# Kernel tuning notes

Hardware: AMD Instinct MI355X
Metric: run time of the kernel (lower is better)

## Reference

```python
import jax, jax.numpy as jnp
import numpy as np

D_MODEL = 1024
NUM_HEADS = 16
HEAD_DIM = D_MODEL // NUM_HEADS
SCALE = 1.0 / np.sqrt(HEAD_DIM).astype(np.float32)


def setup_inputs() -> dict:
    key = jax.random.key(0)
    k1, k2, k3, k4 = jax.random.split(key, 4)
    B, L = 1, 4096
    s = 0.02
    x = jax.random.normal(k1, (B, L, D_MODEL), dtype=jnp.float32)
    W_qkv = jax.random.normal(k2, (D_MODEL, 3 * D_MODEL), dtype=jnp.float32) * s
    W_o = jax.random.normal(k3, (D_MODEL, D_MODEL), dtype=jnp.float32) * s
    b_o = jax.random.normal(k4, (D_MODEL,), dtype=jnp.float32) * s
    return {"x": x, "W_qkv": W_qkv, "W_o": W_o, "b_o": b_o}


def reference(x, W_qkv, W_o, b_o):
    B, L, D = x.shape
    H, Hd = NUM_HEADS, HEAD_DIM
    qkv = x @ W_qkv                          # [B, L, 3D]
    qkv = qkv.reshape(B, L, 3, H, Hd)
    q = jnp.transpose(qkv[:, :, 0], (0, 2, 1, 3))  # [B, H, L, Hd]
    k = jnp.transpose(qkv[:, :, 1], (0, 2, 1, 3))
    v = jnp.transpose(qkv[:, :, 2], (0, 2, 1, 3))
    scores = jnp.einsum("bhqd,bhkd->bhqk", q, k) * SCALE  # [B, H, L, L]
    attn = jax.nn.softmax(scores, axis=-1)
    out = jnp.einsum("bhqk,bhkd->bhqd", attn, v)          # [B, H, L, Hd]
    out = jnp.transpose(out, (0, 2, 1, 3)).reshape(B, L, D)
    return out @ W_o + b_o
```

## Files before the change

### kernel.cpp

```cpp
#include <hip/hip_runtime.h>
#include <stdint.h>


#define L_SEQ 4096
#define DM 1024
#define NHEAD 16
#define HDIM 64
#define ATT_SCALE 0.125f
#define LOG2E 1.4426950408889634f
#define CSC (ATT_SCALE * LOG2E)

typedef __attribute__((ext_vector_type(8))) __bf16 bf16x8;
typedef __attribute__((ext_vector_type(4))) __bf16 bf16x4;
typedef __attribute__((ext_vector_type(4))) float f32x4;
typedef __attribute__((ext_vector_type(8))) float f32x8;
typedef __attribute__((ext_vector_type(4))) short short4v;
typedef __attribute__((ext_vector_type(8))) short short8v;

#define GLL16(g, l) __builtin_amdgcn_global_load_lds( \
    (__attribute__((address_space(1))) void*)(g),     \
    (__attribute__((address_space(3))) void*)(l), 16, 0, 0)

#define MFMA32(a, b, c) __builtin_amdgcn_mfma_f32_16x16x32_bf16((a), (b), (c), 0, 0, 0)

__device__ __forceinline__ short f2bf(float f) {
  uint32_t u = __builtin_bit_cast(uint32_t, f);
  u += 0x7fffu + ((u >> 16) & 1u);
  return (short)(u >> 16);
}

__global__ __launch_bounds__(256)
void prep_kernel(const float* __restrict__ x, short* __restrict__ xb,
                 const float* __restrict__ Wq, short* __restrict__ wqt,
                 const float* __restrict__ Wo, short* __restrict__ wot) {
  __shared__ __align__(16) short tbuf[64 * 66];
  const int tid = threadIdx.x;
  const int blk = blockIdx.x;
  if (blk < 4096) {
    int i = blk * 256 + tid;
    float4 v = ((const float4*)x)[i];
    short4 o;
    o.x = f2bf(v.x); o.y = f2bf(v.y); o.z = f2bf(v.z); o.w = f2bf(v.w);
    ((short4*)xb)[i] = o;
    return;
  }
  const float* W; short* Wt; int N, nb, kb;
  const int K = 1024;
  if (blk < 4096 + 768) {
    int b = blk - 4096;
    W = Wq; Wt = wqt; N = 3072; nb = (b % 48) * 64; kb = (b / 48) * 64;
  } else {
    int b = blk - (4096 + 768);
    W = Wo; Wt = wot; N = 1024; nb = (b % 16) * 64; kb = (b / 16) * 64;
  }
#pragma unroll
  for (int i = 0; i < 16; i++) {
    int idx = tid + i * 256;
    int r = idx >> 6, c = idx & 63;
    tbuf[r * 66 + c] = f2bf(W[(size_t)(kb + r) * N + nb + c]);
  }
  __syncthreads();
#pragma unroll
  for (int i = 0; i < 16; i++) {
    int idx = tid + i * 256;
    int r = idx >> 6, c = idx & 63;
    Wt[(size_t)(nb + r) * K + kb + c] = tbuf[c * 66 + r];
  }
}

__global__ __launch_bounds__(256, 2)
void gemm_qkv(const short* __restrict__ A, const short* __restrict__ Bt,
              short* __restrict__ qkv, short* __restrict__ vtout, int K) {
  __shared__ __align__(16) short As[4096];
  __shared__ __align__(16) short Bs[4096];
  const int tid = threadIdx.x;
  const int lane = tid & 63;
  const int wave = tid >> 6;
  const int quad = lane >> 4;
  const int cl = lane & 15;
  const int m0 = blockIdx.x * 128;
  const int n0 = blockIdx.y * 128;
  const int wm = (wave >> 1) * 64;
  const int wn = (wave & 1) * 64;

  f32x4 acc[4][4] = {};

  for (int kb = 0; kb < K; kb += 32) {
    __syncthreads();
#pragma unroll
    for (int i = 0; i < 2; i++) {
      int ci = i * 256 + tid;
      int row = ci & 127, c = ci >> 7;
      GLL16(A + (size_t)(m0 + row) * K + kb + c * 8, As + ci * 8);
      GLL16(Bt + (size_t)(n0 + row) * K + kb + c * 8, Bs + ci * 8);
    }
    __syncthreads();
    bf16x8 af[4], bfr[4];
#pragma unroll
    for (int t = 0; t < 4; t++) {
      af[t]  = *(const bf16x8*)(As + (quad * 128 + wm + t * 16 + cl) * 8);
      bfr[t] = *(const bf16x8*)(Bs + (quad * 128 + wn + t * 16 + cl) * 8);
    }
#pragma unroll
    for (int mt = 0; mt < 4; mt++)
#pragma unroll
      for (int nt = 0; nt < 4; nt++)
        acc[mt][nt] = MFMA32(af[mt], bfr[nt], acc[mt][nt]);
  }

#pragma unroll
  for (int mt = 0; mt < 4; mt++)
#pragma unroll
    for (int nt = 0; nt < 4; nt++) {
      int col = n0 + wn + nt * 16 + cl;
      int which = col >> 10, hd = col & 63;
      int hidx = (col >> 6) & 15;
      int row0 = m0 + wm + mt * 16 + quad * 4;
      if (which == 2) {
        short4v pk;
#pragma unroll
        for (int r = 0; r < 4; r++) pk[r] = f2bf(acc[mt][nt][r]);
        *(short4v*)(vtout + ((size_t)hidx * HDIM + hd) * L_SEQ + row0) = pk;
      } else {
        float sc = (which == 0) ? CSC : 1.0f;
        size_t base = (((size_t)which * NHEAD + hidx) * L_SEQ) * HDIM + hd;
#pragma unroll
        for (int r = 0; r < 4; r++)
          qkv[base + (size_t)(row0 + r) * HDIM] = f2bf(acc[mt][nt][r] * sc);
      }
    }
}

__global__ __launch_bounds__(256, 2)
void gemm_out(const short* __restrict__ A, const short* __restrict__ Bt,
              float* __restrict__ C, const float* __restrict__ bias, int K) {
  __shared__ __align__(16) short As[4096];
  __shared__ __align__(16) short Bs[2048];
  const int tid = threadIdx.x;
  const int lane = tid & 63;
  const int wave = tid >> 6;
  const int quad = lane >> 4;
  const int cl = lane & 15;
  const int m0 = blockIdx.x * 128;
  const int n0 = blockIdx.y * 64;
  const int wm = (wave >> 1) * 64;
  const int wn = (wave & 1) * 32;
  const int N = 1024;

  f32x4 acc[4][2] = {};

  for (int kb = 0; kb < K; kb += 32) {
    __syncthreads();
#pragma unroll
    for (int i = 0; i < 2; i++) {
      int ci = i * 256 + tid;
      GLL16(A + (size_t)(m0 + (ci & 127)) * K + kb + (ci >> 7) * 8, As + ci * 8);
    }
    GLL16(Bt + (size_t)(n0 + (tid & 63)) * K + kb + (tid >> 6) * 8, Bs + tid * 8);
    __syncthreads();
    bf16x8 af[4], bfr[2];
#pragma unroll
    for (int t = 0; t < 4; t++)
      af[t] = *(const bf16x8*)(As + (quad * 128 + wm + t * 16 + cl) * 8);
#pragma unroll
    for (int t = 0; t < 2; t++)
      bfr[t] = *(const bf16x8*)(Bs + (quad * 64 + wn + t * 16 + cl) * 8);
#pragma unroll
    for (int mt = 0; mt < 4; mt++)
#pragma unroll
      for (int nt = 0; nt < 2; nt++)
        acc[mt][nt] = MFMA32(af[mt], bfr[nt], acc[mt][nt]);
  }

#pragma unroll
  for (int mt = 0; mt < 4; mt++)
#pragma unroll
    for (int nt = 0; nt < 2; nt++) {
      int col = n0 + wn + nt * 16 + cl;
      float b = bias[col];
#pragma unroll
      for (int r = 0; r < 4; r++) {
        int row = m0 + wm + mt * 16 + quad * 4 + r;
        C[(size_t)row * N + col] = acc[mt][nt][r] + b;
      }
    }
}

#define KVB 128
__global__ __launch_bounds__(512, 4)
void attn_kernel(const short* __restrict__ qkv, const short* __restrict__ vt,
                 short* __restrict__ aout) {
  __shared__ __align__(16) short Ks[2][KVB * HDIM];
  __shared__ __align__(16) short Vs[2][HDIM * KVB];
  __shared__ float lbuf[512];
  const int tid = threadIdx.x, lane = tid & 63, wave = tid >> 6;
  const int quad = lane >> 4, cl = lane & 15;
  const int kg = wave & 1;
  const int qg = wave >> 1;
  const int bid = blockIdx.x;
  const int h  = ((bid & 7) << 1) | ((bid >> 3) & 1);
  const int qb = bid >> 4;
  const short* Qg = qkv + (size_t)h * L_SEQ * HDIM;
  const short* Kg = qkv + ((size_t)NHEAD + h) * L_SEQ * HDIM;
  const short* Vg = vt + (size_t)h * HDIM * L_SEQ;
  const int keyoff = ((cl >> 2) << 3) | (cl & 3);

  bf16x8 qf[2][2];
#pragma unroll
  for (int qs = 0; qs < 2; qs++) {
    int qrow = qb * 128 + qg * 32 + qs * 16 + cl;
    qf[qs][0] = *(const bf16x8*)(Qg + (size_t)qrow * HDIM + quad * 8);
    qf[qs][1] = *(const bf16x8*)(Qg + (size_t)qrow * HDIM + 32 + quad * 8);
  }
  const short8v ov = {0x3F80, 0x3F80, 0x3F80, 0x3F80, 0x3F80, 0x3F80, 0x3F80, 0x3F80};
  const bf16x8 ones = __builtin_bit_cast(bf16x8, ov);
  f32x4 o_l[2] = {};
  f32x4 o_acc[4][2] = {};

  int koff[2][2][2];
  int voff[2][4];
#pragma unroll
  for (int kslab = 0; kslab < 2; kslab++) {
#pragma unroll
    for (int b = 0; b < 2; b++) {
      int krow = kg * 64 + kslab * 32 + keyoff + b * 4;
      int sw = (krow & 3) | (((krow >> 3) & 1) << 2);
#pragma unroll
      for (int ks = 0; ks < 2; ks++)
        koff[kslab][b][ks] = (krow * 8 + ((ks * 4 + quad) ^ sw)) * 8;
    }
#pragma unroll
    for (int G = 0; G < 4; G++) {
      int vrow = G * 16 + cl;
      int sw = (vrow & 3) | (((vrow >> 3) & 1) << 2);
      voff[kslab][G] = (vrow * 16 + ((kg * 8 + kslab * 4 + quad) ^ sw)) * 8;
    }
  }

  const short* kp[2]; const short* vp[2]; int ldsoK[2], ldsoV[2];
#pragma unroll
  for (int i = 0; i < 2; i++) {
    int ciK = i * 512 + tid;
    int rowK = ciK >> 3;
    int swK = (rowK & 3) | (((rowK >> 3) & 1) << 2);
    int cK = (ciK & 7) ^ swK;
    kp[i] = Kg + (size_t)rowK * HDIM + cK * 8;
    ldsoK[i] = ciK * 8;
    int ciV = i * 512 + tid;
    int rowV = ciV >> 4;
    int swV = (rowV & 3) | (((rowV >> 3) & 1) << 2);
    int cV = (ciV & 15) ^ swV;
    vp[i] = Vg + (size_t)rowV * L_SEQ + cV * 8;
    ldsoV[i] = ciV * 8;
  }
#define STAGE(t, buf)                                        \
  {                                                          \
    _Pragma("unroll")                                        \
    for (int i = 0; i < 2; i++) {                            \
      GLL16(kp[i] + (t) * KVB * HDIM, &Ks[buf][ldsoK[i]]);   \
      GLL16(vp[i] + (t) * KVB, &Vs[buf][ldsoV[i]]);          \
    }                                                        \
  }

  STAGE(0, 0);
#pragma unroll 2
  for (int t = 0; t < L_SEQ / KVB; t++) {
    const int cur = t & 1;
    __syncthreads();
    if (t + 1 < L_SEQ / KVB) STAGE(t + 1, cur ^ 1);
    const short* Kb = Ks[cur];
    const short* Vb = Vs[cur];

#pragma unroll
    for (int kslab = 0; kslab < 2; kslab++) {
      f32x4 s[2][2] = {};
      __builtin_amdgcn_s_setprio(1);
#pragma unroll
      for (int b = 0; b < 2; b++)
#pragma unroll
        for (int ks = 0; ks < 2; ks++) {
          bf16x8 kf = *(const bf16x8*)(Kb + koff[kslab][b][ks]);
#pragma unroll
          for (int qs = 0; qs < 2; qs++)
            s[qs][b] = MFMA32(kf, qf[qs][ks], s[qs][b]);
        }
      __builtin_amdgcn_s_setprio(0);

      bf16x8 vfr[4];
#pragma unroll
      for (int G = 0; G < 4; G++)
        vfr[G] = *(const bf16x8*)(Vb + voff[kslab][G]);

      bf16x8 pb0;
      {
        f32x8 pv8;
#pragma unroll
        for (int b = 0; b < 2; b++)
#pragma unroll
          for (int r = 0; r < 4; r++)
            pv8[b * 4 + r] = __builtin_amdgcn_exp2f(s[0][b][r]);
        pb0 = __builtin_convertvector(pv8, bf16x8);
      }

      __builtin_amdgcn_s_setprio(1);
      o_l[0] = MFMA32(ones, pb0, o_l[0]);
#pragma unroll
      for (int G = 0; G < 4; G++)
        o_acc[G][0] = MFMA32(vfr[G], pb0, o_acc[G][0]);
      __builtin_amdgcn_s_setprio(0);

      bf16x8 pb1;
      {
        f32x8 pv8;
#pragma unroll
        for (int b = 0; b < 2; b++)
#pragma unroll
          for (int r = 0; r < 4; r++)
            pv8[b * 4 + r] = __builtin_amdgcn_exp2f(s[1][b][r]);
        pb1 = __builtin_convertvector(pv8, bf16x8);
      }

      __builtin_amdgcn_s_setprio(1);
      o_l[1] = MFMA32(ones, pb1, o_l[1]);
#pragma unroll
      for (int G = 0; G < 4; G++)
        o_acc[G][1] = MFMA32(vfr[G], pb1, o_acc[G][1]);
      __builtin_amdgcn_s_setprio(0);
    }
  }
#undef STAGE

  __syncthreads();
  float* ored = (float*)&Ks[0][0];
  if (kg == 1) {
#pragma unroll
    for (int G = 0; G < 4; G++)
#pragma unroll
      for (int qs = 0; qs < 2; qs++)
        *(f32x4*)&ored[(((qg * 4 + G) * 2 + qs) * 64 + lane) * 4] = o_acc[G][qs];
#pragma unroll
    for (int qs = 0; qs < 2; qs++)
      lbuf[(qg * 2 + qs) * 64 + lane] = o_l[qs][0];
  }
  __syncthreads();
  if (kg == 0) {
#pragma unroll
    for (int qs = 0; qs < 2; qs++) {
      float l = o_l[qs][0] + lbuf[(qg * 2 + qs) * 64 + lane];
      float inv = 1.f / l;
      int token = qb * 128 + qg * 32 + qs * 16 + cl;
#pragma unroll
      for (int G = 0; G < 4; G++) {
        f32x4 part = *(const f32x4*)&ored[(((qg * 4 + G) * 2 + qs) * 64 + lane) * 4];
        f32x4 sc = (o_acc[G][qs] + part) * inv;
        bf16x4 pk = __builtin_convertvector(sc, bf16x4);
        *(short4v*)(aout + (size_t)token * DM + h * HDIM + G * 16 + quad * 4) =
            __builtin_bit_cast(short4v, pk);
      }
    }
  }
}

extern "C" void kernel_launch(void* const* d_in, const int* in_sizes, int n_in,
                              void* d_out, int out_size, void* d_ws, size_t ws_size,
                              hipStream_t stream) {
  const float* x    = (const float*)d_in[0];
  const float* Wqkv = (const float*)d_in[1];
  const float* Wo   = (const float*)d_in[2];
  const float* bo   = (const float*)d_in[3];
  char* ws = (char*)d_ws;
  short* xb    = (short*)(ws);
  short* wqkvt = (short*)(ws + (size_t)8 * 1024 * 1024);
  short* wot   = (short*)(ws + (size_t)14 * 1024 * 1024);
  short* qkv   = (short*)(ws + (size_t)16 * 1024 * 1024);
  short* vt    = (short*)(ws + (size_t)40 * 1024 * 1024);
  short* aout  = xb;
  float* out = (float*)d_out;

  prep_kernel<<<4096 + 768 + 256, 256, 0, stream>>>(x, xb, Wqkv, wqkvt, Wo, wot);
  gemm_qkv<<<dim3(32, 24), 256, 0, stream>>>(xb, wqkvt, qkv, vt, DM);
  attn_kernel<<<dim3(512), 512, 0, stream>>>(qkv, vt, aout);
  gemm_out<<<dim3(32, 16), 256, 0, stream>>>(aout, wot, out, bo, DM);
}
```

Baseline: 233.2 us.

## Deepen QKV GEMM K-step, stage Q/K epilogue via LDS, re-layout V tile

The QKV projection GEMM now loads 64-wide K slabs per barrier pair instead of 32, halving the number of synchronisations per tile. Its Q/K epilogue first transposes the accumulators through shared memory, then writes 16-byte vectorised rows to global memory instead of scattered 2-byte stores. The V-tile LDS layout in the attention kernel is also changed to split each row by key half, with matching swizzle and read offsets. LDS per block doubles, which may affect occupancy, and the epilogue adds extra barriers.

```diff
diff --git a/kernel.cpp b/kernel.cpp
--- a/kernel.cpp
+++ b/kernel.cpp
@@ -71,8 +71,9 @@
 __global__ __launch_bounds__(256, 2)
 void gemm_qkv(const short* __restrict__ A, const short* __restrict__ Bt,
               short* __restrict__ qkv, short* __restrict__ vtout, int K) {
-  __shared__ __align__(16) short As[4096];
-  __shared__ __align__(16) short Bs[4096];
+  __shared__ __align__(16) short smem[16384];
+  short* As = smem;
+  short* Bs = smem + 8192;
   const int tid = threadIdx.x;
   const int lane = tid & 63;
   const int wave = tid >> 6;
@@ -85,50 +86,77 @@
 
   f32x4 acc[4][4] = {};
 
-  for (int kb = 0; kb < K; kb += 32) {
+  for (int kb = 0; kb < K; kb += 64) {
     __syncthreads();
 #pragma unroll
-    for (int i = 0; i < 2; i++) {
+    for (int i = 0; i < 4; i++) {
       int ci = i * 256 + tid;
       int row = ci & 127, c = ci >> 7;
       GLL16(A + (size_t)(m0 + row) * K + kb + c * 8, As + ci * 8);
       GLL16(Bt + (size_t)(n0 + row) * K + kb + c * 8, Bs + ci * 8);
     }
     __syncthreads();
-    bf16x8 af[4], bfr[4];
-#pragma unroll
-    for (int t = 0; t < 4; t++) {
-      af[t]  = *(const bf16x8*)(As + (quad * 128 + wm + t * 16 + cl) * 8);
-      bfr[t] = *(const bf16x8*)(Bs + (quad * 128 + wn + t * 16 + cl) * 8);
-    }
+#pragma unroll
+    for (int ks = 0; ks < 2; ks++) {
+      bf16x8 af[4], bfr[4];
+#pragma unroll
+      for (int t = 0; t < 4; t++) {
+        af[t]  = *(const bf16x8*)(As + ((ks * 4 + quad) * 128 + wm + t * 16 + cl) * 8);
+        bfr[t] = *(const bf16x8*)(Bs + ((ks * 4 + quad) * 128 + wn + t * 16 + cl) * 8);
+      }
+#pragma unroll
+      for (int mt = 0; mt < 4; mt++)
+#pragma unroll
+        for (int nt = 0; nt < 4; nt++)
+          acc[mt][nt] = MFMA32(af[mt], bfr[nt], acc[mt][nt]);
+    }
+  }
+
+  const int which = n0 >> 10;
+  if (which == 2) {
 #pragma unroll
     for (int mt = 0; mt < 4; mt++)
 #pragma unroll
-      for (int nt = 0; nt < 4; nt++)
-        acc[mt][nt] = MFMA32(af[mt], bfr[nt], acc[mt][nt]);
-  }
-
-#pragma unroll
-  for (int mt = 0; mt < 4; mt++)
-#pragma unroll
-    for (int nt = 0; nt < 4; nt++) {
-      int col = n0 + wn + nt * 16 + cl;
-      int which = col >> 10, hd = col & 63;
-      int hidx = (col >> 6) & 15;
-      int row0 = m0 + wm + mt * 16 + quad * 4;
-      if (which == 2) {
+      for (int nt = 0; nt < 4; nt++) {
+        int col = n0 + wn + nt * 16 + cl;
+        int hd = col & 63;
+        int hidx = (col >> 6) & 15;
+        int row0 = m0 + wm + mt * 16 + quad * 4;
         short4v pk;
 #pragma unroll
         for (int r = 0; r < 4; r++) pk[r] = f2bf(acc[mt][nt][r]);
         *(short4v*)(vtout + ((size_t)hidx * HDIM + hd) * L_SEQ + row0) = pk;
-      } else {
-        float sc = (which == 0) ? CSC : 1.0f;
-        size_t base = (((size_t)which * NHEAD + hidx) * L_SEQ) * HDIM + hd;
-#pragma unroll
-        for (int r = 0; r < 4; r++)
-          qkv[base + (size_t)(row0 + r) * HDIM] = f2bf(acc[mt][nt][r] * sc);
-      }
-    }
+      }
+  } else {
+    const float sc = (which == 0) ? CSC : 1.0f;
+    short* Ct = smem;
+#pragma unroll
+    for (int p = 0; p < 2; p++) {
+      __syncthreads();
+      if ((wave & 1) == p) {
+#pragma unroll
+        for (int mt = 0; mt < 4; mt++)
+#pragma unroll
+          for (int nt = 0; nt < 4; nt++) {
+            int m = wm + mt * 16 + quad * 4;
+            int c = nt * 16 + cl;
+#pragma unroll
+            for (int r = 0; r < 4; r++)
+              Ct[(m + r) * 72 + c] = f2bf(acc[mt][nt][r] * sc);
+          }
+      }
+      __syncthreads();
+      int hidx = ((n0 + p * 64) >> 6) & 15;
+      size_t base = ((size_t)which * NHEAD + hidx) * L_SEQ * HDIM;
+      int m = tid >> 1;
+      int j0 = (tid & 1) * 4;
+#pragma unroll
+      for (int i = 0; i < 4; i++) {
+        short8v v = *(const short8v*)(Ct + m * 72 + (j0 + i) * 8);
+        *(short8v*)(qkv + base + (size_t)(m0 + m) * HDIM + (j0 + i) * 8) = v;
+      }
+    }
+  }
 }
 
 __global__ __launch_bounds__(256, 2)
@@ -233,7 +261,7 @@
     for (int G = 0; G < 4; G++) {
       int vrow = G * 16 + cl;
       int sw = (vrow & 3) | (((vrow >> 3) & 1) << 2);
-      voff[kslab][G] = (vrow * 16 + ((kg * 8 + kslab * 4 + quad) ^ sw)) * 8;
+      voff[kslab][G] = ((kg * 64 + vrow) * 8 + ((kslab * 4 + quad) ^ sw)) * 8;
     }
   }
 
@@ -247,10 +275,11 @@
     kp[i] = Kg + (size_t)rowK * HDIM + cK * 8;
     ldsoK[i] = ciK * 8;
     int ciV = i * 512 + tid;
-    int rowV = ciV >> 4;
-    int swV = (rowV & 3) | (((rowV >> 3) & 1) << 2);
-    int cV = (ciV & 15) ^ swV;
-    vp[i] = Vg + (size_t)rowV * L_SEQ + cV * 8;
+    int half = ciV >> 9;
+    int hd = (ciV >> 3) & 63;
+    int cp = ciV & 7;
+    int swV = (hd & 3) | (((hd >> 3) & 1) << 2);
+    vp[i] = Vg + (size_t)hd * L_SEQ + (half * 8 + (cp ^ swV)) * 8;
     ldsoV[i] = ciV * 8;
   }
 #define STAGE(t, buf)                                        \
```

New measurement: 236.7 us. About the same (+1.5%).
